# Optimization experiments

Hardware: AMD Instinct MI355X
Metric: run time of the kernel (lower is better)

## Reference

```python
import jax, jax.numpy as jnp
import numpy as np
from jax import lax

HEADS = 8
DIM_HEAD = 64
INNER = HEADS * DIM_HEAD  # 512
DIM = 256
TOP_K = 512  # top_k=-1 -> Lk // heads = 4096 // 8
LN_EPS = 1e-5


def chan_ln(x, g, b):
    # LayerNorm over channel dim (axis=1) of [b,c,D,H,W]
    mu = jnp.mean(x, axis=1, keepdims=True)
    var = jnp.mean((x - mu) ** 2, axis=1, keepdims=True)
    xn = (x - mu) * lax.rsqrt(var + LN_EPS)
    return xn * g[None, :, None, None, None] + b[None, :, None, None, None]


def l1_cdist(K, Q):
    # K: [B,N,D], Q: [B,M,D] -> [B,N,M]; scan over feature dim to avoid a [B,N,M,D] intermediate
    Kt = jnp.moveaxis(K, -1, 0)  # [D,B,N]
    Qt = jnp.moveaxis(Q, -1, 0)  # [D,B,M]
    acc0 = jnp.zeros((K.shape[0], K.shape[1], Q.shape[1]), K.dtype)
    def step(acc, kq):
        kd, qd = kq
        return acc + jnp.abs(kd[:, :, None] - qd[:, None, :]), None
    acc, _ = lax.scan(step, acc0, (Kt, Qt))
    return acc


def l2norm_ax(t, axis):
    n = jnp.sqrt(jnp.sum(t * t, axis=axis, keepdims=True))
    return t / jnp.maximum(n, 1e-12)


def setup_inputs() -> dict:
    key = jax.random.key(0)
    ks = jax.random.split(key, 12)
    b, Dq, Hq, Wq = 2, 16, 32, 32
    Dc, Hc, Wc = 16, 16, 16
    Lk = Dc * Hc * Wc  # 4096
    return {
        "query_source": jax.random.normal(ks[0], (b, DIM, Dq, Hq, Wq), jnp.float32),
        "context": jax.random.normal(ks[1], (b, DIM, Dc, Hc, Wc), jnp.float32),
        "rand_idx": jax.random.randint(ks[2], (b * HEADS, TOP_K), 0, 4096),
        "g_ctx": jnp.ones((DIM,), jnp.float32),
        "b_ctx": jnp.zeros((DIM,), jnp.float32),
        "g_qs": jnp.ones((DIM,), jnp.float32),
        "b_qs": jnp.zeros((DIM,), jnp.float32),
        "w_kv": jax.random.normal(ks[3], (2 * INNER, DIM), jnp.float32) * 0.02,
        "w_q": jax.random.normal(ks[4], (INNER, DIM), jnp.float32) * 0.02,
        "w_out": jax.random.normal(ks[5], (DIM, INNER), jnp.float32) * 0.02,
        "g_out": jnp.ones((DIM,), jnp.float32),
        "b_out": jnp.zeros((DIM,), jnp.float32),
        "gamma": jnp.full((1,), 0.5, jnp.float32),
    }


def reference(query_source, context, rand_idx, g_ctx, b_ctx, g_qs, b_qs,
              w_kv, w_q, w_out, g_out, b_out, gamma):
    b, c, Dq, Hq, Wq = query_source.shape
    Lq = Dq * Hq * Wq
    Lk = context.shape[2] * context.shape[3] * context.shape[4]

    ctx = chan_ln(context, g_ctx, b_ctx)
    qsn = chan_ln(query_source, g_qs, b_qs)

    # 1x1x1 convs == channel matmuls
    kv = jnp.einsum('oc,bcdhw->bodhw', w_kv, ctx)
    k, v = jnp.split(kv, 2, axis=1)
    q = jnp.einsum('oc,bcdhw->bodhw', w_q, qsn)

    def fold(t):  # [b, inner, ...] -> [b, heads, dim_head, L]
        return t.reshape(t.shape[0], HEADS, DIM_HEAD, -1)
    q, k, v = fold(q), fold(k), fold(v)
    # l2norm over dim_head channels (torch dim=1 after (b h) fold)
    q = l2norm_ax(q, 2)
    k = l2norm_ax(k, 2)
    # -> [b, heads, L, dim_head]
    q = jnp.swapaxes(q, 2, 3)
    k = jnp.swapaxes(k, 2, 3)
    v = jnp.swapaxes(v, 2, 3)

    BH = b * HEADS
    qf = q.reshape(BH, Lq, DIM_HEAD)
    kf = k.reshape(BH, Lk, DIM_HEAD)
    vf = v.reshape(BH, Lk, DIM_HEAD)

    # random-query-anchored token pruning
    Q_small = jnp.take_along_axis(qf, rand_idx[:, :, None], axis=1)  # [BH, TOP_K, dh]
    dist = l1_cdist(kf, Q_small)                                     # [BH, Lk, TOP_K]
    min_d = jnp.min(dist, axis=2)                                    # [BH, Lk]
    _, idx = lax.top_k(-min_d, TOP_K)                                # smallest distances
    ks_sel = jnp.take_along_axis(kf, idx[:, :, None], axis=1)        # [BH, TOP_K, dh]
    vs_sel = jnp.take_along_axis(vf, idx[:, :, None], axis=1)

    ks4 = ks_sel.reshape(b, HEADS, TOP_K, DIM_HEAD)
    vs4 = vs_sel.reshape(b, HEADS, TOP_K, DIM_HEAD)

    # SDPA with scale=1.0, no dropout (eval)
    scores = jnp.einsum('bhqd,bhkd->bhqk', q, ks4)
    attn = jax.nn.softmax(scores, axis=-1)
    out = jnp.einsum('bhqk,bhkd->bhqd', attn, vs4)  # [b,H,Lq,dh]

    out = out.reshape(b, HEADS, Dq, Hq, Wq, DIM_HEAD)
    out = jnp.transpose(out, (0, 1, 5, 2, 3, 4)).reshape(b, INNER, Dq, Hq, Wq)
    out = jnp.einsum('oc,bcdhw->bodhw', w_out, out)
    out = chan_ln(out, g_out, b_out)
    return gamma[0] * out + query_source
```

## Files before the change

kernel.cpp:

```cpp
#include <hip/hip_runtime.h>
#include <hip/hip_bf16.h>
#include <math.h>

#define DIMC  256
#define HEADS 8
#define DH    64
#define INNER 512
#define TOPK  512
#define LQ    16384
#define LKE   4096
#define NB    2
#define NBH   16

typedef __attribute__((ext_vector_type(8))) short bf16x8;
typedef __attribute__((ext_vector_type(4))) float f32x4;
typedef __attribute__((ext_vector_type(16))) unsigned u32x16;

__device__ __forceinline__ unsigned short f2bf(float f) {
    unsigned u = __float_as_uint(f);
    u += 0x7FFFu + ((u >> 16) & 1u);
    return (unsigned short)(u >> 16);
}
__device__ __forceinline__ float bf2f(unsigned short b) {
    return __uint_as_float(((unsigned)b) << 16);
}
__device__ __forceinline__ f32x4 mfma16(bf16x8 a, bf16x8 b, f32x4 c) {
    return __builtin_amdgcn_mfma_f32_16x16x32_bf16(a, b, c, 0, 0, 0);
}
__device__ __forceinline__ unsigned f2q16(float v) {
    return (unsigned)((int)rintf(v * 32000.0f) + 32768) & 0xFFFFu;
}

__global__ void stats_kernel(const float* __restrict__ x, float* __restrict__ mu,
                             float* __restrict__ rs, int L, int total) {
    int idx = blockIdx.x * 256 + threadIdx.x;
    if (idx >= total) return;
    int b = idx / L, l = idx - b * L;
    const float* p = x + (size_t)b * DIMC * L + l;
    float s = 0.f, sq = 0.f;
    for (int c = 0; c < DIMC; c++) {
        float v = p[(size_t)c * L];
        s += v; sq += v * v;
    }
    float m = s * (1.0f / DIMC);
    float var = fmaxf(sq * (1.0f / DIMC) - m * m, 0.f);
    mu[idx] = m;
    rs[idx] = rsqrtf(var + 1e-5f);
}

template<bool WRITELO>
__global__ __launch_bounds__(256) void ln_transpose_kernel(
    const float* __restrict__ x, const float* __restrict__ mu, const float* __restrict__ rs,
    const float* __restrict__ g, const float* __restrict__ beta, int L,
    unsigned short* __restrict__ xhi, unsigned short* __restrict__ xlo) {
    int lt = blockIdx.x, ct = blockIdx.y, b = blockIdx.z;
    int l0 = lt * 64, c0 = ct * 64;
    int t = threadIdx.x;
    __shared__ float T[64][65];
#pragma unroll
    for (int r = 0; r < 16; r++) {
        int f = r * 256 + t;
        int l = f & 63, c = f >> 6;
        int loc = b * L + l0 + l;
        float v = x[((size_t)b * DIMC + c0 + c) * L + l0 + l];
        T[c][l] = (v - mu[loc]) * rs[loc] * g[c0 + c] + beta[c0 + c];
    }
    __syncthreads();
#pragma unroll
    for (int r = 0; r < 16; r++) {
        int f = r * 256 + t;
        int c = f & 63, l = f >> 6;
        float v = T[c][l];
        unsigned short hi = f2bf(v);
        size_t di = ((size_t)b * L + l0 + l) * DIMC + c0 + c;
        xhi[di] = hi;
        if (WRITELO) xlo[di] = f2bf(v - bf2f(hi));
    }
}

template<int MODE>
__global__ __launch_bounds__(256) void gemm_mfma_kernel(
    const float* __restrict__ wmat,
    const unsigned short* __restrict__ xhi, const unsigned short* __restrict__ xlo,
    void* __restrict__ dst0, void* __restrict__ dst1, void* __restrict__ dst2) {
    constexpr int K = (MODE == 2) ? 512 : 256;
    constexpr int N = (MODE == 0) ? LKE : LQ;
    constexpr bool MAYSPLIT = (MODE == 0);
    int n0 = blockIdx.x * 128;
    int by = blockIdx.y;
    int bb = blockIdx.z;
    int t = threadIdx.x, w = t >> 6, lane = t & 63;
    int wm = w >> 1, wn = w & 1;
    int lanelo = lane & 15, lanehi = lane >> 4;

    __shared__ __align__(16) char Wh[16384];
    __shared__ __align__(16) char Xh[16384];
    __shared__ __align__(16) char Wl[MAYSPLIT ? 16384 : 16];
    __shared__ __align__(16) char Xl[MAYSPLIT ? 16384 : 16];

    bool split = MAYSPLIT && (by < 4);

    const float* wsrc = wmat + (size_t)by * 128 * K;
    const unsigned short* xsh = xhi + ((size_t)bb * N + n0) * K;
    const unsigned short* xsl = xlo + ((size_t)bb * N + n0) * K;

    f32x4 acc[4][4];
#pragma unroll
    for (int mi = 0; mi < 4; mi++)
#pragma unroll
        for (int ni = 0; ni < 4; ni++) acc[mi][ni] = (f32x4){0.f, 0.f, 0.f, 0.f};

    for (int k0 = 0; k0 < K; k0 += 64) {
        if (k0) __syncthreads();
#pragma unroll
        for (int gg = 0; gg < 4; gg++) {
            int e = gg * 2048 + t * 8;
            int row = e >> 6, kc = e & 63;
            const float* wp = wsrc + (size_t)row * K + k0 + kc;
            bf16x8 hi, lo;
#pragma unroll
            for (int i = 0; i < 8; i++) {
                float v = wp[i];
                unsigned short h = f2bf(v);
                hi[i] = (short)h;
                if (MAYSPLIT) lo[i] = (short)f2bf(v - bf2f(h));
            }
            int off = (row * 128 + kc * 2) ^ ((row & 7) << 4);
            *(bf16x8*)(Wh + off) = hi;
            *(bf16x8*)(Xh + off) = *(const bf16x8*)(xsh + (size_t)row * K + k0 + kc);
            if (split) {
                *(bf16x8*)(Wl + off) = lo;
                *(bf16x8*)(Xl + off) = *(const bf16x8*)(xsl + (size_t)row * K + k0 + kc);
            }
        }
        __syncthreads();
#pragma unroll
        for (int kk = 0; kk < 2; kk++) {
            bf16x8 ah[4], bh_[4];
#pragma unroll
            for (int mi = 0; mi < 4; mi++) {
                int row = wm * 64 + mi * 16 + lanelo;
                int off = (row * 128 + kk * 64 + lanehi * 16) ^ ((row & 7) << 4);
                ah[mi] = *(const bf16x8*)(Wh + off);
            }
#pragma unroll
            for (int ni = 0; ni < 4; ni++) {
                int row = wn * 64 + ni * 16 + lanelo;
                int off = (row * 128 + kk * 64 + lanehi * 16) ^ ((row & 7) << 4);
                bh_[ni] = *(const bf16x8*)(Xh + off);
            }
#pragma unroll
            for (int mi = 0; mi < 4; mi++)
#pragma unroll
                for (int ni = 0; ni < 4; ni++)
                    acc[mi][ni] = mfma16(ah[mi], bh_[ni], acc[mi][ni]);
            if (split) {
                bf16x8 al[4], bl_[4];
#pragma unroll
                for (int mi = 0; mi < 4; mi++) {
                    int row = wm * 64 + mi * 16 + lanelo;
                    int off = (row * 128 + kk * 64 + lanehi * 16) ^ ((row & 7) << 4);
                    al[mi] = *(const bf16x8*)(Wl + off);
                }
#pragma unroll
                for (int ni = 0; ni < 4; ni++) {
                    int row = wn * 64 + ni * 16 + lanelo;
                    int off = (row * 128 + kk * 64 + lanehi * 16) ^ ((row & 7) << 4);
                    bl_[ni] = *(const bf16x8*)(Xl + off);
                }
#pragma unroll
                for (int mi = 0; mi < 4; mi++)
#pragma unroll
                    for (int ni = 0; ni < 4; ni++) {
                        acc[mi][ni] = mfma16(ah[mi], bl_[ni], acc[mi][ni]);
                        acc[mi][ni] = mfma16(al[mi], bh_[ni], acc[mi][ni]);
                    }
            }
        }
    }

    bool donorm = (MODE == 1) || (MODE == 0 && by < 4);
    float inv[4];
    if (donorm) {
#pragma unroll
        for (int ni = 0; ni < 4; ni++) {
            float s = 0.f;
#pragma unroll
            for (int mi = 0; mi < 4; mi++)
#pragma unroll
                for (int rg = 0; rg < 4; rg++) s += acc[mi][ni][rg] * acc[mi][ni][rg];
            s += __shfl_xor(s, 16);
            s += __shfl_xor(s, 32);
            inv[ni] = 1.0f / fmaxf(sqrtf(s), 1e-12f);
        }
    }
#pragma unroll
    for (int mi = 0; mi < 4; mi++) {
        int rowg = by * 128 + wm * 64 + mi * 16 + lanehi * 4;
#pragma unroll
        for (int ni = 0; ni < 4; ni++) {
            int l = n0 + wn * 64 + ni * 16 + lanelo;
            if (MODE == 0) {
                bool isk = rowg < 512;
                float sc = isk ? inv[ni] : 1.0f;
                int h = (rowg >> 6) & 7, d0 = rowg & 63;
                float4 v = make_float4(acc[mi][ni][0] * sc, acc[mi][ni][1] * sc,
                                       acc[mi][ni][2] * sc, acc[mi][ni][3] * sc);
                float* dp = isk ? (float*)dst0 : (float*)dst1;
                size_t base = ((size_t)(bb * HEADS + h) * LKE + l) * 64 + d0;
                *(float4*)&dp[base] = v;
                if (isk) {
                    uint2 pk;
                    pk.x = f2q16(v.x) | (f2q16(v.y) << 16);
                    pk.y = f2q16(v.z) | (f2q16(v.w) << 16);
                    *(uint2*)&((unsigned*)dst2)[(((size_t)(bb * HEADS + h) * LKE + l) * 64 + d0) / 2] = pk;
                }
            } else if (MODE == 1) {
                int h = rowg >> 6, d0 = rowg & 63;
                ushort4 u;
                u.x = f2bf(acc[mi][ni][0] * inv[ni]);
                u.y = f2bf(acc[mi][ni][1] * inv[ni]);
                u.z = f2bf(acc[mi][ni][2] * inv[ni]);
                u.w = f2bf(acc[mi][ni][3] * inv[ni]);
                unsigned short* qp = (unsigned short*)dst0;
                *(ushort4*)&qp[((size_t)(bb * HEADS + h) * LQ + l) * 64 + d0] = u;
            } else {
                float4 v = make_float4(acc[mi][ni][0], acc[mi][ni][1],
                                       acc[mi][ni][2], acc[mi][ni][3]);
                float* pp = (float*)dst0;
                *(float4*)&pp[((size_t)bb * LQ + l) * 256 + rowg] = v;
            }
        }
    }
}

__global__ __launch_bounds__(256) void qsample_kernel(
    const float* __restrict__ x, const float* __restrict__ mu, const float* __restrict__ rs,
    const float* __restrict__ g, const float* __restrict__ beta,
    const float* __restrict__ w, const int* __restrict__ ridx,
    unsigned* __restrict__ Qint) {
    int lt = blockIdx.x, bh = blockIdx.y;
    int b = bh >> 3, h = bh & 7;
    int t = threadIdx.x, tx = t & 15, ty = t >> 4;
    __shared__ float Ws[64][33];
    __shared__ float Xs[32][65];
    __shared__ float Cs[64][65];
    __shared__ float nf[64];
    __shared__ int lidx[64];
    if (t < 64) lidx[t] = ridx[bh * TOPK + lt * 64 + t];
    __syncthreads();
    float acc[4][4];
#pragma unroll
    for (int a = 0; a < 4; a++)
#pragma unroll
        for (int c2 = 0; c2 < 4; c2++) acc[a][c2] = 0.f;
    for (int kc = 0; kc < DIMC; kc += 32) {
#pragma unroll
        for (int r = 0; r < 8; r++) {
            int f = r * 256 + t;
            int oi = f >> 5, kj = f & 31;
            Ws[oi][kj] = w[(size_t)(h * 64 + oi) * DIMC + kc + kj];
        }
#pragma unroll
        for (int r = 0; r < 8; r++) {
            int f = r * 256 + t;
            int kj = f >> 6, lj = f & 63;
            int l = lidx[lj];
            int loc = b * LQ + l;
            float v = x[(size_t)b * DIMC * LQ + (size_t)(kc + kj) * LQ + l];
            Xs[kj][lj] = (v - mu[loc]) * rs[loc] * g[kc + kj] + beta[kc + kj];
        }
        __syncthreads();
#pragma unroll
        for (int kj = 0; kj < 32; kj++) {
            float wr[4], xr[4];
#pragma unroll
            for (int a = 0; a < 4; a++) wr[a] = Ws[ty * 4 + a][kj];
#pragma unroll
            for (int c2 = 0; c2 < 4; c2++) xr[c2] = Xs[kj][tx * 4 + c2];
#pragma unroll
            for (int a = 0; a < 4; a++)
#pragma unroll
                for (int c2 = 0; c2 < 4; c2++) acc[a][c2] += wr[a] * xr[c2];
        }
        __syncthreads();
    }
#pragma unroll
    for (int a = 0; a < 4; a++)
#pragma unroll
        for (int c2 = 0; c2 < 4; c2++) Cs[ty * 4 + a][tx * 4 + c2] = acc[a][c2];
    __syncthreads();
    if (t < 64) {
        float sq = 0.f;
        for (int o = 0; o < 64; o++) { float v = Cs[o][t]; sq += v * v; }
        nf[t] = 1.0f / fmaxf(sqrtf(sq), 1e-12f);
    }
    __syncthreads();
#pragma unroll
    for (int r = 0; r < 8; r++) {
        int f = r * 256 + t;
        int dp = f & 31, lj = f >> 5;
        float v0 = Cs[dp * 2][lj] * nf[lj];
        float v1 = Cs[dp * 2 + 1][lj] * nf[lj];
        Qint[((size_t)bh * TOPK + (size_t)lt * 64 + lj) * 32 + dp] =
            f2q16(v0) | (f2q16(v1) << 16);
    }
}

__global__ __launch_bounds__(256) __attribute__((amdgpu_waves_per_eu(4, 4)))
void cdist_sad_kernel(
    const unsigned* __restrict__ kint,
    const unsigned* __restrict__ Qint,
    unsigned* __restrict__ min_d4) {
    int bh = blockIdx.y;
    int key = blockIdx.x * 256 + threadIdx.x;
    int qz = blockIdx.z;
    const unsigned* kp = kint + ((size_t)bh * LKE + key) * 32;
    unsigned k[32];
#pragma unroll
    for (int d8 = 0; d8 < 8; d8++) {
        uint4 v = *(const uint4*)(kp + d8 * 4);
        k[d8 * 4 + 0] = v.x; k[d8 * 4 + 1] = v.y;
        k[d8 * 4 + 2] = v.z; k[d8 * 4 + 3] = v.w;
    }
#pragma unroll
    for (int d = 0; d < 32; d++) asm volatile("" : "+v"(k[d]));

    unsigned long long qaddr = (unsigned long long)(const void*)
        (Qint + ((size_t)bh * TOPK + (size_t)qz * (TOPK / 4)) * 32);
    u32x16 qa0, qa1, qb0, qb1;
    asm volatile(
        "s_load_dwordx16 %0, %2, 0x00\n\t"
        "s_load_dwordx16 %1, %2, 0x40"
        : "=s"(qa0), "=s"(qa1) : "s"(qaddr));
    unsigned best = 0xFFFFFFFFu;

#define S1(ACC, KK, QQ) asm("v_sad_u16 %0, %1, %2, %0" : "+v"(ACC) : "v"(KK), "s"(QQ));
#define S16(QV, KB) \
    S1(a0, k[KB + 0], QV[0])  S1(a1, k[KB + 1], QV[1]) \
    S1(a2, k[KB + 2], QV[2])  S1(a3, k[KB + 3], QV[3]) \
    S1(a0, k[KB + 4], QV[4])  S1(a1, k[KB + 5], QV[5]) \
    S1(a2, k[KB + 6], QV[6])  S1(a3, k[KB + 7], QV[7]) \
    S1(a0, k[KB + 8], QV[8])  S1(a1, k[KB + 9], QV[9]) \
    S1(a2, k[KB + 10], QV[10]) S1(a3, k[KB + 11], QV[11]) \
    S1(a0, k[KB + 12], QV[12]) S1(a1, k[KB + 13], QV[13]) \
    S1(a2, k[KB + 14], QV[14]) S1(a3, k[KB + 15], QV[15])

    for (int qi = 0; qi < TOPK / 4; qi += 2) {
        asm volatile(
            "s_load_dwordx16 %0, %2, 0x80\n\t"
            "s_load_dwordx16 %1, %2, 0xc0"
            : "=s"(qb0), "=s"(qb1) : "s"(qaddr));
        asm volatile("s_waitcnt lgkmcnt(2)" : "+s"(qa0), "+s"(qa1));
        {
            unsigned a0 = 0, a1 = 0, a2 = 0, a3 = 0;
            S16(qa0, 0) S16(qa1, 16)
            best = min(best, (a0 + a1) + (a2 + a3));
        }
        qaddr += 256;
        asm volatile(
            "s_load_dwordx16 %0, %2, 0x00\n\t"
            "s_load_dwordx16 %1, %2, 0x40"
            : "=s"(qa0), "=s"(qa1) : "s"(qaddr));
        asm volatile("s_waitcnt lgkmcnt(2)" : "+s"(qb0), "+s"(qb1));
        {
            unsigned a0 = 0, a1 = 0, a2 = 0, a3 = 0;
            S16(qb0, 0) S16(qb1, 16)
            best = min(best, (a0 + a1) + (a2 + a3));
        }
    }
#undef S16
#undef S1
    min_d4[((size_t)qz * NBH + bh) * LKE + key] = best;
}

__global__ void select_topk_kernel(const unsigned* __restrict__ min_d4, int* __restrict__ isel) {
    int bh = blockIdx.x;
    int t = threadIdx.x;
    __shared__ unsigned su[LKE];
    __shared__ int hist[256];
    __shared__ int sb[2];
    for (int i = t; i < LKE; i += 256) {
        unsigned a = min(min_d4[(size_t)bh * LKE + i],
                         min_d4[(size_t)(NBH + bh) * LKE + i]);
        unsigned b = min(min_d4[(size_t)(2 * NBH + bh) * LKE + i],
                         min_d4[(size_t)(3 * NBH + bh) * LKE + i]);
        su[i] = min(a, b);
    }
    unsigned prefix = 0, mask = 0;
    int need = TOPK;
    for (int shift = 24; shift >= 0; shift -= 8) {
        hist[t] = 0;
        __syncthreads();
        for (int i = t; i < LKE; i += 256) {
            unsigned u = su[i];
            if ((u & mask) == prefix) atomicAdd(&hist[(u >> shift) & 255], 1);
        }
        __syncthreads();
        if (t == 0) {
            int c = 0, bsel = 0;
            for (; bsel < 255; bsel++) {
                if (c + hist[bsel] >= need) break;
                c += hist[bsel];
            }
            sb[0] = bsel; sb[1] = need - c;
        }
        __syncthreads();
        prefix |= ((unsigned)sb[0]) << shift;
        mask |= (255u << shift);
        need = sb[1];
        __syncthreads();
    }
    if (t < 64) {
        int pos = 0, eqseen = 0;
        unsigned long long lanem1 = (t == 0) ? 0ull : ((1ull << t) - 1ull);
        for (int i0 = 0; i0 < LKE; i0 += 64) {
            unsigned u = su[i0 + t];
            bool lt = (u < prefix);
            bool eq = (u == prefix);
            unsigned long long be = __ballot(eq);
            int eqbefore = __popcll(be & lanem1);
            bool take = lt || (eq && (eqseen + eqbefore) < need);
            unsigned long long bt = __ballot(take);
            if (take) isel[bh * TOPK + pos + __popcll(bt & lanem1)] = i0 + t;
            pos += __popcll(bt);
            eqseen += __popcll(be);
        }
    }
}

__global__ void gather_k_kernel(const float* __restrict__ kf, const int* __restrict__ isel,
                                unsigned short* __restrict__ kselh) {
    int idx = blockIdx.x * 256 + threadIdx.x;
    int d = idx & 63;
    int ti = (idx >> 6) & (TOPK - 1);
    int bh = idx >> 15;
    int row = isel[bh * TOPK + ti];
    kselh[idx] = f2bf(kf[((size_t)bh * LKE + row) * 64 + d]);
}

__global__ __launch_bounds__(256) void gather_vT_kernel(
    const float* __restrict__ vf, const int* __restrict__ isel,
    unsigned short* __restrict__ vTh) {
    int bh = blockIdx.y, kc = blockIdx.x * 64;
    int t = threadIdx.x;
    __shared__ float T[64][65];
#pragma unroll
    for (int r = 0; r < 4; r++) {
        int c = r * 256 + t;
        int row = c >> 4, c4 = c & 15;
        int krow = isel[bh * TOPK + kc + row];
        float4 v = *(const float4*)(vf + ((size_t)bh * LKE + krow) * 64 + c4 * 4);
        T[row][c4 * 4 + 0] = v.x; T[row][c4 * 4 + 1] = v.y;
        T[row][c4 * 4 + 2] = v.z; T[row][c4 * 4 + 3] = v.w;
    }
    __syncthreads();
#pragma unroll
    for (int r = 0; r < 16; r++) {
        int f = r * 256 + t;
        int d = f >> 6, key = f & 63;
        vTh[(size_t)bh * 64 * TOPK + (size_t)d * TOPK + kc + key] = f2bf(T[key][d]);
    }
}

__global__ __launch_bounds__(256) void attn_mfma_kernel(
    const unsigned short* __restrict__ qh,
    const unsigned short* __restrict__ kselh,
    const unsigned short* __restrict__ vTh,
    unsigned short* __restrict__ afT) {
    int bh = blockIdx.y, rt = blockIdx.x;
    int bq = bh >> 3, h = bh & 7;
    int t = threadIdx.x, w = t >> 6, lane = t & 63;
    __shared__ unsigned short Qs[64 * 64];
    __shared__ unsigned short Ks[64 * 64];
    __shared__ unsigned short Vts[64 * 64];
    __shared__ unsigned short Ps[4 * 16 * 64];

    const unsigned short* qb = qh + ((size_t)bh * LQ + (size_t)rt * 64) * 64;
    const unsigned short* kb = kselh + (size_t)bh * TOPK * 64;
    const unsigned short* vb = vTh + (size_t)bh * 64 * TOPK;

#pragma unroll
    for (int r = 0; r < 2; r++) {
        int c = r * 256 + t; int row = c >> 3, c8 = c & 7;
        bf16x8 v = *(const bf16x8*)(qb + row * 64 + c8 * 8);
        *(bf16x8*)((char*)Qs + ((row * 128 + c8 * 16) ^ ((row & 7) << 4))) = v;
    }
    auto stageKV = [&](int kc0) {
#pragma unroll
        for (int r = 0; r < 2; r++) {
            int c = r * 256 + t; int row = c >> 3, c8 = c & 7;
            int off = (row * 128 + c8 * 16) ^ ((row & 7) << 4);
            *(bf16x8*)((char*)Ks + off) = *(const bf16x8*)(kb + (kc0 + row) * 64 + c8 * 8);
            *(bf16x8*)((char*)Vts + off) = *(const bf16x8*)(vb + row * TOPK + kc0 + c8 * 8);
        }
    };
    stageKV(0);
    __syncthreads();

    bf16x8 qfrag[2];
#pragma unroll
    for (int kk = 0; kk < 2; kk++) {
        int row = w * 16 + (lane & 15);
        qfrag[kk] = *(const bf16x8*)((char*)Qs +
            ((row * 128 + kk * 64 + (lane >> 4) * 16) ^ ((row & 7) << 4)));
    }

    f32x4 o[4];
#pragma unroll
    for (int m = 0; m < 4; m++) o[m] = (f32x4){0.f, 0.f, 0.f, 0.f};
    float lsum[4] = {0.f, 0.f, 0.f, 0.f};
    unsigned short* pw = Ps + w * 16 * 64;

    for (int ch = 0; ch < 8; ch++) {
        f32x4 s[4];
#pragma unroll
        for (int n = 0; n < 4; n++) {
            s[n] = (f32x4){0.f, 0.f, 0.f, 0.f};
#pragma unroll
            for (int kk = 0; kk < 2; kk++) {
                int row = n * 16 + (lane & 15);
                bf16x8 kfr = *(const bf16x8*)((char*)Ks +
                    ((row * 128 + kk * 64 + (lane >> 4) * 16) ^ ((row & 7) << 4)));
                s[n] = mfma16(qfrag[kk], kfr, s[n]);
            }
        }
        float part[4] = {0.f, 0.f, 0.f, 0.f};
#pragma unroll
        for (int n = 0; n < 4; n++) {
#pragma unroll
            for (int rg = 0; rg < 4; rg++) {
                float p = __expf(s[n][rg]);
                part[rg] += p;
                int row = (lane >> 4) * 4 + rg, col = n * 16 + (lane & 15);
                *(unsigned short*)((char*)pw +
                    ((row * 128 + col * 2) ^ ((row & 7) << 4))) = f2bf(p);
            }
        }
#pragma unroll
        for (int rg = 0; rg < 4; rg++) {
            float v = part[rg];
            v += __shfl_xor(v, 1); v += __shfl_xor(v, 2);
            v += __shfl_xor(v, 4); v += __shfl_xor(v, 8);
            lsum[rg] += v;
        }
        bf16x8 pfrag[2];
#pragma unroll
        for (int kk = 0; kk < 2; kk++) {
            int row = lane & 15;
            pfrag[kk] = *(const bf16x8*)((char*)pw +
                ((row * 128 + kk * 64 + (lane >> 4) * 16) ^ ((row & 7) << 4)));
        }
#pragma unroll
        for (int m = 0; m < 4; m++) {
#pragma unroll
            for (int kk = 0; kk < 2; kk++) {
                int row = m * 16 + (lane & 15);
                bf16x8 vfr = *(const bf16x8*)((char*)Vts +
                    ((row * 128 + kk * 64 + (lane >> 4) * 16) ^ ((row & 7) << 4)));
                o[m] = mfma16(pfrag[kk], vfr, o[m]);
            }
        }
        if (ch < 7) {
            __syncthreads();
            stageKV((ch + 1) * 64);
            __syncthreads();
        }
    }
    int row0 = w * 16 + (lane >> 4) * 4;
#pragma unroll
    for (int rg = 0; rg < 4; rg++) {
        float invs = 1.0f / lsum[rg];
        int l = rt * 64 + row0 + rg;
        size_t base = ((size_t)bq * LQ + l) * 512 + h * 64 + (lane & 15);
#pragma unroll
        for (int m = 0; m < 4; m++)
            afT[base + m * 16] = f2bf(o[m][rg] * invs);
    }
}

__global__ void stats_loc_kernel(const float* __restrict__ pre, float* __restrict__ mu,
                                 float* __restrict__ rs) {
    int t = threadIdx.x;
    int grp = t >> 4, ln = t & 15;
    int loc = blockIdx.x * 16 + grp;
    const float4* p = (const float4*)(pre + (size_t)loc * 256);
    float s = 0.f, sq = 0.f;
#pragma unroll
    for (int i = 0; i < 4; i++) {
        float4 v = p[ln + i * 16];
        s += v.x + v.y + v.z + v.w;
        sq += v.x * v.x + v.y * v.y + v.z * v.z + v.w * v.w;
    }
#pragma unroll
    for (int d = 1; d < 16; d <<= 1) {
        s += __shfl_xor(s, d);
        sq += __shfl_xor(sq, d);
    }
    if (ln == 0) {
        float m = s * (1.0f / 256.0f);
        float var = fmaxf(sq * (1.0f / 256.0f) - m * m, 0.f);
        mu[loc] = m;
        rs[loc] = rsqrtf(var + 1e-5f);
    }
}

__global__ __launch_bounds__(256) void final_kernel(
    const float* __restrict__ pre, const float* __restrict__ mu,
    const float* __restrict__ rs, const float* __restrict__ g,
    const float* __restrict__ beta, const float* __restrict__ gamma,
    const float* __restrict__ qs_in, float* __restrict__ out) {
    int lt = blockIdx.x, ot = blockIdx.y, b = blockIdx.z;
    int l0 = lt * 64, o0 = ot * 64;
    int t = threadIdx.x;
    __shared__ float T[64][65];
    float gm = gamma[0];
#pragma unroll
    for (int r = 0; r < 16; r++) {
        int f = r * 256 + t;
        int o = f & 63, l = f >> 6;
        int loc = b * LQ + l0 + l;
        float v = pre[(size_t)loc * 256 + o0 + o];
        T[o][l] = ((v - mu[loc]) * rs[loc] * g[o0 + o] + beta[o0 + o]) * gm;
    }
    __syncthreads();
#pragma unroll
    for (int r = 0; r < 16; r++) {
        int f = r * 256 + t;
        int l = f & 63, o = f >> 6;
        size_t oi = ((size_t)(b * DIMC + o0 + o)) * LQ + l0 + l;
        out[oi] = T[o][l] + qs_in[oi];
    }
}

extern "C" void kernel_launch(void* const* d_in, const int* in_sizes, int n_in,
                              void* d_out, int out_size, void* d_ws, size_t ws_size,
                              hipStream_t stream) {
    const float* qs_in = (const float*)d_in[0];
    const float* ctx   = (const float*)d_in[1];
    const int*   ridx  = (const int*)d_in[2];
    const float* g_ctx = (const float*)d_in[3];
    const float* b_ctx = (const float*)d_in[4];
    const float* g_qs  = (const float*)d_in[5];
    const float* b_qs  = (const float*)d_in[6];
    const float* w_kv  = (const float*)d_in[7];
    const float* w_q   = (const float*)d_in[8];
    const float* w_out = (const float*)d_in[9];
    const float* g_out = (const float*)d_in[10];
    const float* b_out = (const float*)d_in[11];
    const float* gamma = (const float*)d_in[12];
    float* out = (float*)d_out;

    char* ws = (char*)d_ws;
    size_t off = 0;
    auto alloc = [&](size_t bytes) { char* p = ws + off; off += (bytes + 255) & ~(size_t)255; return p; };

    float*          kf    = (float*)alloc((size_t)NBH * LKE * 64 * 4);
    float*          vf    = (float*)alloc((size_t)NBH * LKE * 64 * 4);
    unsigned*       kint  = (unsigned*)alloc((size_t)NBH * LKE * 32 * 4);
    unsigned short* qh    = (unsigned short*)alloc((size_t)NBH * LQ * 64 * 2);
    char*           uni   = alloc((size_t)NB * LQ * INNER * 2);
    unsigned short* ctxT_hi = (unsigned short*)(uni);
    unsigned short* ctxT_lo = (unsigned short*)(uni + (size_t)NB * LKE * DIMC * 2);
    unsigned short* qsT_hi  = (unsigned short*)(uni + (size_t)2 * NB * LKE * DIMC * 2);
    unsigned short* afT     = (unsigned short*)(uni);

    unsigned*       Qint  = (unsigned*)alloc((size_t)NBH * TOPK * 32 * 4);
    unsigned short* kselh = (unsigned short*)alloc((size_t)NBH * TOPK * 64 * 2);
    unsigned short* vTh   = (unsigned short*)alloc((size_t)NBH * 64 * TOPK * 2);
    float*          pre   = (float*)alloc((size_t)NB * LQ * DIMC * 4);
    unsigned*       min_d4= (unsigned*)alloc((size_t)4 * NBH * LKE * 4);
    float*          mu_c  = (float*)alloc(NB * LKE * 4);
    float*          rs_c  = (float*)alloc(NB * LKE * 4);
    float*          mu_q  = (float*)alloc(NB * LQ * 4);
    float*          rs_q  = (float*)alloc(NB * LQ * 4);
    float*          mu_o  = (float*)alloc(NB * LQ * 4);
    float*          rs_o  = (float*)alloc(NB * LQ * 4);
    int*            isel  = (int*)alloc(NBH * TOPK * 4);

    stats_kernel<<<(NB * LKE + 255) / 256, 256, 0, stream>>>(ctx, mu_c, rs_c, LKE, NB * LKE);
    stats_kernel<<<(NB * LQ + 255) / 256, 256, 0, stream>>>(qs_in, mu_q, rs_q, LQ, NB * LQ);
    ln_transpose_kernel<true><<<dim3(LKE / 64, DIMC / 64, NB), 256, 0, stream>>>(
        ctx, mu_c, rs_c, g_ctx, b_ctx, LKE, ctxT_hi, ctxT_lo);
    ln_transpose_kernel<false><<<dim3(LQ / 64, DIMC / 64, NB), 256, 0, stream>>>(
        qs_in, mu_q, rs_q, g_qs, b_qs, LQ, qsT_hi, nullptr);
    gemm_mfma_kernel<0><<<dim3(LKE / 128, 8, NB), 256, 0, stream>>>(
        w_kv, ctxT_hi, ctxT_lo, kf, vf, kint);
    gemm_mfma_kernel<1><<<dim3(LQ / 128, 4, NB), 256, 0, stream>>>(
        w_q, qsT_hi, qsT_hi, qh, nullptr, nullptr);
    qsample_kernel<<<dim3(TOPK / 64, NBH), 256, 0, stream>>>(
        qs_in, mu_q, rs_q, g_qs, b_qs, w_q, ridx, Qint);
    cdist_sad_kernel<<<dim3(LKE / 256, NBH, 4), 256, 0, stream>>>(kint, Qint, min_d4);
    select_topk_kernel<<<NBH, 256, 0, stream>>>(min_d4, isel);
    gather_k_kernel<<<(NBH * TOPK * 64) / 256, 256, 0, stream>>>(kf, isel, kselh);
    gather_vT_kernel<<<dim3(TOPK / 64, NBH), 256, 0, stream>>>(vf, isel, vTh);
    attn_mfma_kernel<<<dim3(LQ / 64, NBH), 256, 0, stream>>>(qh, kselh, vTh, afT);
    gemm_mfma_kernel<2><<<dim3(LQ / 128, 2, NB), 256, 0, stream>>>(
        w_out, afT, afT, pre, nullptr, nullptr);
    stats_loc_kernel<<<(NB * LQ) / 16, 256, 0, stream>>>(pre, mu_o, rs_o);
    final_kernel<<<dim3(LQ / 64, DIMC / 64, NB), 256, 0, stream>>>(
        pre, mu_o, rs_o, g_out, b_out, gamma, qs_in, out);
}
```

Measured before the change: 352.1 us.

## Double-buffer K/V tiles in attention kernel with register prefetch

The attention kernel now keeps two LDS buffers for K and V. Each chunk's next tile is loaded into registers before the MFMA work and written to the alternate buffer afterwards, which cuts the two barriers per chunk down to one and hides global load latency behind compute. The per-row softmax sum reduction is also moved out of the loop, so the lane shuffles run once at the end. In exchange the kernel uses more LDS and registers, which could reduce occupancy.

```diff
diff --git a/kernel.cpp b/kernel.cpp
--- a/kernel.cpp
+++ b/kernel.cpp
@@ -472,30 +472,35 @@
     int bq = bh >> 3, h = bh & 7;
     int t = threadIdx.x, w = t >> 6, lane = t & 63;
     __shared__ unsigned short Qs[64 * 64];
-    __shared__ unsigned short Ks[64 * 64];
-    __shared__ unsigned short Vts[64 * 64];
+    __shared__ unsigned short Ks[2][64 * 64];
+    __shared__ unsigned short Vts[2][64 * 64];
     __shared__ unsigned short Ps[4 * 16 * 64];
 
     const unsigned short* qb = qh + ((size_t)bh * LQ + (size_t)rt * 64) * 64;
     const unsigned short* kb = kselh + (size_t)bh * TOPK * 64;
     const unsigned short* vb = vTh + (size_t)bh * 64 * TOPK;
 
-#pragma unroll
-    for (int r = 0; r < 2; r++) {
-        int c = r * 256 + t; int row = c >> 3, c8 = c & 7;
-        bf16x8 v = *(const bf16x8*)(qb + row * 64 + c8 * 8);
-        *(bf16x8*)((char*)Qs + ((row * 128 + c8 * 16) ^ ((row & 7) << 4))) = v;
-    }
-    auto stageKV = [&](int kc0) {
-#pragma unroll
-        for (int r = 0; r < 2; r++) {
-            int c = r * 256 + t; int row = c >> 3, c8 = c & 7;
-            int off = (row * 128 + c8 * 16) ^ ((row & 7) << 4);
-            *(bf16x8*)((char*)Ks + off) = *(const bf16x8*)(kb + (kc0 + row) * 64 + c8 * 8);
-            *(bf16x8*)((char*)Vts + off) = *(const bf16x8*)(vb + row * TOPK + kc0 + c8 * 8);
-        }
-    };
-    stageKV(0);
+    int row0s = t >> 3, c80 = t & 7;
+    int row1s = 32 + (t >> 3), c81 = t & 7;
+    int offs0 = (row0s * 128 + c80 * 16) ^ ((row0s & 7) << 4);
+    int offs1 = (row1s * 128 + c81 * 16) ^ ((row1s & 7) << 4);
+
+    {
+        bf16x8 v0 = *(const bf16x8*)(qb + row0s * 64 + c80 * 8);
+        bf16x8 v1 = *(const bf16x8*)(qb + row1s * 64 + c81 * 8);
+        *(bf16x8*)((char*)Qs + offs0) = v0;
+        *(bf16x8*)((char*)Qs + offs1) = v1;
+    }
+    {
+        bf16x8 k0 = *(const bf16x8*)(kb + row0s * 64 + c80 * 8);
+        bf16x8 k1 = *(const bf16x8*)(kb + row1s * 64 + c81 * 8);
+        bf16x8 v0 = *(const bf16x8*)(vb + row0s * TOPK + c80 * 8);
+        bf16x8 v1 = *(const bf16x8*)(vb + row1s * TOPK + c81 * 8);
+        *(bf16x8*)((char*)Ks[0] + offs0) = k0;
+        *(bf16x8*)((char*)Ks[0] + offs1) = k1;
+        *(bf16x8*)((char*)Vts[0] + offs0) = v0;
+        *(bf16x8*)((char*)Vts[0] + offs1) = v1;
+    }
     __syncthreads();
 
     bf16x8 qfrag[2];
@@ -509,10 +514,19 @@
     f32x4 o[4];
 #pragma unroll
     for (int m = 0; m < 4; m++) o[m] = (f32x4){0.f, 0.f, 0.f, 0.f};
-    float lsum[4] = {0.f, 0.f, 0.f, 0.f};
+    float part[4] = {0.f, 0.f, 0.f, 0.f};
     unsigned short* pw = Ps + w * 16 * 64;
+    int cur = 0;
 
     for (int ch = 0; ch < 8; ch++) {
+        bf16x8 knx0, knx1, vnx0, vnx1;
+        if (ch < 7) {
+            int kc0 = (ch + 1) * 64;
+            knx0 = *(const bf16x8*)(kb + (kc0 + row0s) * 64 + c80 * 8);
+            knx1 = *(const bf16x8*)(kb + (kc0 + row1s) * 64 + c81 * 8);
+            vnx0 = *(const bf16x8*)(vb + row0s * TOPK + kc0 + c80 * 8);
+            vnx1 = *(const bf16x8*)(vb + row1s * TOPK + kc0 + c81 * 8);
+        }
         f32x4 s[4];
 #pragma unroll
         for (int n = 0; n < 4; n++) {
@@ -520,12 +534,11 @@
 #pragma unroll
             for (int kk = 0; kk < 2; kk++) {
                 int row = n * 16 + (lane & 15);
-                bf16x8 kfr = *(const bf16x8*)((char*)Ks +
+                bf16x8 kfr = *(const bf16x8*)((char*)Ks[cur] +
                     ((row * 128 + kk * 64 + (lane >> 4) * 16) ^ ((row & 7) << 4)));
                 s[n] = mfma16(qfrag[kk], kfr, s[n]);
             }
         }
-        float part[4] = {0.f, 0.f, 0.f, 0.f};
 #pragma unroll
         for (int n = 0; n < 4; n++) {
 #pragma unroll
@@ -537,13 +550,6 @@
                     ((row * 128 + col * 2) ^ ((row & 7) << 4))) = f2bf(p);
             }
         }
-#pragma unroll
-        for (int rg = 0; rg < 4; rg++) {
-            float v = part[rg];
-            v += __shfl_xor(v, 1); v += __shfl_xor(v, 2);
-            v += __shfl_xor(v, 4); v += __shfl_xor(v, 8);
-            lsum[rg] += v;
-        }
         bf16x8 pfrag[2];
 #pragma unroll
         for (int kk = 0; kk < 2; kk++) {
@@ -556,16 +562,27 @@
 #pragma unroll
             for (int kk = 0; kk < 2; kk++) {
                 int row = m * 16 + (lane & 15);
-                bf16x8 vfr = *(const bf16x8*)((char*)Vts +
+                bf16x8 vfr = *(const bf16x8*)((char*)Vts[cur] +
                     ((row * 128 + kk * 64 + (lane >> 4) * 16) ^ ((row & 7) << 4)));
                 o[m] = mfma16(pfrag[kk], vfr, o[m]);
             }
         }
         if (ch < 7) {
-            __syncthreads();
-            stageKV((ch + 1) * 64);
-            __syncthreads();
-        }
+            *(bf16x8*)((char*)Ks[cur ^ 1] + offs0) = knx0;
+            *(bf16x8*)((char*)Ks[cur ^ 1] + offs1) = knx1;
+            *(bf16x8*)((char*)Vts[cur ^ 1] + offs0) = vnx0;
+            *(bf16x8*)((char*)Vts[cur ^ 1] + offs1) = vnx1;
+        }
+        __syncthreads();
+        cur ^= 1;
+    }
+    float lsum[4];
+#pragma unroll
+    for (int rg = 0; rg < 4; rg++) {
+        float v = part[rg];
+        v += __shfl_xor(v, 1); v += __shfl_xor(v, 2);
+        v += __shfl_xor(v, 4); v += __shfl_xor(v, 8);
+        lsum[rg] = v;
     }
     int row0 = w * 16 + (lane >> 4) * 4;
 #pragma unroll
```

Measured after the change: 343.8 us. 1.02x faster.
